# Performance work log

Measured on AMD Instinct MI355X. Metric: run time of the kernel, lower is better.

Reference implementation:

```python
import jax, jax.numpy as jnp
import numpy as np

N = 100000   # nodes
E = 1600000  # edges (before self loops)
H = 4        # heads
C = 32       # per-head channels
D = H * C    # hidden_dim = 128
G = 64       # graphs in batch
L = 4        # num_layers
IN_DIM = 7
NEG_SLOPE = 0.2


def setup_inputs() -> dict:
    key = jax.random.key(0)
    ks = jax.random.split(key, 14)
    s = 0.1
    x = jax.random.normal(ks[0], (N, IN_DIM), jnp.float32)
    edge_index = jax.random.randint(ks[1], (2, E), 0, N, dtype=jnp.int32)
    batch = jnp.sort(jax.random.randint(ks[2], (N,), 0, G, dtype=jnp.int32))
    W0 = jax.random.normal(ks[3], (IN_DIM, D), jnp.float32) * s
    a_src0 = jax.random.normal(ks[4], (H, C), jnp.float32) * s
    a_dst0 = jax.random.normal(ks[5], (H, C), jnp.float32) * s
    b0 = jnp.zeros((D,), jnp.float32)
    Ws = jax.random.normal(ks[6], (L - 1, D, D), jnp.float32) * s
    a_srcs = jax.random.normal(ks[7], (L - 1, H, C), jnp.float32) * s
    a_dsts = jax.random.normal(ks[8], (L - 1, H, C), jnp.float32) * s
    bs = jnp.zeros((L - 1, D), jnp.float32)
    ln_g = jnp.ones((L, D), jnp.float32)
    ln_b = jnp.zeros((L, D), jnp.float32)
    return dict(x=x, edge_index=edge_index, batch=batch, W0=W0, a_src0=a_src0,
                a_dst0=a_dst0, b0=b0, Ws=Ws, a_srcs=a_srcs, a_dsts=a_dsts,
                bs=bs, ln_g=ln_g, ln_b=ln_b)


def _gat_layer(x, W, a_src, a_dst, b, src, dst):
    # x: [N, F_in] -> h: [N, H, C] (PyG GATConv: shared lin for src/dst)
    h = (x @ W).reshape(N, H, C)
    alpha_src = jnp.einsum('nhc,hc->nh', h, a_src)  # [N, H]
    alpha_dst = jnp.einsum('nhc,hc->nh', h, a_dst)  # [N, H]
    logits = jax.nn.leaky_relu(alpha_src[src] + alpha_dst[dst], NEG_SLOPE)  # [E', H]
    # segment softmax over edges grouped by destination node
    m = jax.ops.segment_max(logits, dst, num_segments=N)          # [N, H]
    e = jnp.exp(logits - m[dst])
    z = jax.ops.segment_sum(e, dst, num_segments=N)               # [N, H]
    alpha = e / (z[dst] + 1e-16)                                  # [E', H]
    msg = h[src] * alpha[..., None]                               # [E', H, C]
    out = jax.ops.segment_sum(msg, dst, num_segments=N)           # [N, H, C]
    return out.reshape(N, D) + b


def _layernorm(x, g, b):
    mu = jnp.mean(x, axis=-1, keepdims=True)
    var = jnp.var(x, axis=-1, keepdims=True)
    return (x - mu) * jax.lax.rsqrt(var + 1e-5) * g + b


def reference(x, edge_index, batch, W0, a_src0, a_dst0, b0, Ws, a_srcs, a_dsts, bs, ln_g, ln_b):
    # PyG GATConv default: add self loops
    loop = jnp.arange(N, dtype=edge_index.dtype)
    src = jnp.concatenate([edge_index[0], loop])
    dst = jnp.concatenate([edge_index[1], loop])
    h = x
    for i in range(L):
        if i == 0:
            W, asr, ads, b = W0, a_src0, a_dst0, b0
        else:
            W, asr, ads, b = Ws[i - 1], a_srcs[i - 1], a_dsts[i - 1], bs[i - 1]
        h_new = _gat_layer(h, W, asr, ads, b, src, dst)
        h_new = jax.nn.elu(_layernorm(h_new, ln_g[i], ln_b[i]))
        h = h + h_new if i > 0 else h_new  # dropout is identity in eval
    node_embeddings = h  # [N, D]
    sums = jax.ops.segment_sum(node_embeddings, batch, num_segments=G)  # [G, D]
    cnt = jax.ops.segment_sum(jnp.ones((N,), node_embeddings.dtype), batch, num_segments=G)
    graph_embedding = sums / jnp.maximum(cnt, 1.0)[:, None]
    return node_embeddings, graph_embedding
```

## Files before the change

kernel.cpp:

```cpp
#include <hip/hip_runtime.h>
#include <hip/hip_bf16.h>

#define NN 100000
#define NE 1600000
#define NH 4
#define NC 32
#define DD 128
#define NG 64
#define NIN 7

#define BSH 9
#define NBUK ((NN + 511) >> BSH)
#define SEGCAP 9600
#define CAPE (SEGCAP - 512)
#define CSRN (NBUK * SEGCAP)
#define NBBIN ((NE + 4095)/4096)

typedef __hip_bfloat16 bf16;
typedef __attribute__((ext_vector_type(8))) short short8;
typedef __attribute__((ext_vector_type(4))) float f32x4;
typedef __attribute__((ext_vector_type(2))) float f32x2;

__device__ __forceinline__ float b2f(const bf16 v){ return __bfloat162float(v); }

__device__ __forceinline__ float in_ld(const void* p, size_t i, int f32){
  return f32 ? ((const float*)p)[i] : b2f(((const bf16*)p)[i]);
}

__device__ __forceinline__ unsigned int bfbits(float v){
  bf16 b = __float2bfloat16(v);
  return (unsigned int)(*(unsigned short*)&b);
}

__global__ __launch_bounds__(256) void k_init(float* __restrict__ gsum, int* __restrict__ gcnt,
                                              int* __restrict__ bcur,
                                              const unsigned int* __restrict__ xb, int* __restrict__ flag){
  int i = blockIdx.x*256 + threadIdx.x;
  if (i < NG*DD) gsum[i] = 0.f;
  if (i < NG) gcnt[i] = 0;
  if (i < NBUK) bcur[i] = i * CAPE;
  if (blockIdx.x == 0 && threadIdx.x < 64){
    int t = threadIdx.x;
    int pl = 0;
    for (int j = t; j < 512; j += 64){
      float v = __uint_as_float(xb[j]);
      float a = fabsf(v);
      if (v == v && a < 1e6f && a > 1e-10f) pl++;
    }
    #pragma unroll
    for (int off = 32; off > 0; off >>= 1) pl += __shfl_down(pl, off);
    if (t == 0) *flag = (pl >= 384) ? 1 : 0;
  }
}

__global__ __launch_bounds__(256) void k_bin(const int* __restrict__ src, const int* __restrict__ dst,
                                             int* __restrict__ bcur, int2* __restrict__ gstag,
                                             const void* __restrict__ Ws, bf16* __restrict__ WT,
                                             const int* __restrict__ flag){
  if (blockIdx.x >= NBBIN){
    int l = blockIdx.x - NBBIN;
    int f32 = *flag;
    for (int idx = threadIdx.x; idx < DD*DD; idx += 256){
      int n = idx >> 7, k = idx & 127;
      WT[(size_t)l*DD*DD + idx] = __float2bfloat16(in_ld(Ws, (size_t)l*DD*DD + (size_t)k*DD + n, f32));
    }
    return;
  }
  __shared__ int cnt[NBUK], pref[NBUK+1], place[NBUK], gbase[NBUK];
  __shared__ int2 pairs[4096];
  int tid = threadIdx.x;
  for (int b = tid; b < NBUK; b += 256){ cnt[b]=0; place[b]=0; }
  __syncthreads();
  int e0 = blockIdx.x*4096;
  int s[16], d[16];
  #pragma unroll
  for (int i=0;i<16;i++){
    int e = e0 + i*256 + tid;
    s[i] = 0; d[i] = -1;
    if (e < NE){
      unsigned int us = (unsigned int)src[e]; if (us >= NN) us = 0;
      unsigned int ud = (unsigned int)dst[e]; if (ud >= NN) ud = 0;
      s[i] = (int)us; d[i] = (int)ud;
      atomicAdd(&cnt[ud>>BSH], 1);
    }
  }
  __syncthreads();
  if (tid == 0){
    int run = 0;
    for (int b=0;b<NBUK;b++){ pref[b] = run; run += cnt[b]; }
    pref[NBUK] = run;
  }
  __syncthreads();
  for (int b = tid; b < NBUK; b += 256){
    if (cnt[b] > 0) gbase[b] = atomicAdd(&bcur[b], cnt[b]);
  }
  __syncthreads();
  #pragma unroll
  for (int i=0;i<16;i++){
    if (d[i] >= 0){
      int b = d[i]>>BSH;
      int lp = atomicAdd(&place[b],1);
      pairs[pref[b]+lp] = make_int2(s[i], d[i]);
    }
  }
  __syncthreads();
  int tot = pref[NBUK];
  for (int j = tid; j < tot; j += 256){
    int2 pr = pairs[j];
    int b = pr.y>>BSH;
    int gidx = gbase[b] + (j - pref[b]);
    if (gidx >= b*CAPE && gidx < (b+1)*CAPE) gstag[gidx] = pr;
  }
}

__global__ __launch_bounds__(256) void k_bucket(const int2* __restrict__ gstag,
                                                const int* __restrict__ bcur,
                                                int* __restrict__ csr,
                                                int* __restrict__ offs, int* __restrict__ oend){
  __shared__ int seg[SEGCAP];
  __shared__ int lcnt[512];
  __shared__ int loff[512];
  __shared__ int pscan[256];
  int b = blockIdx.x, tid = threadIdx.x;
  int nstart = b << BSH;
  int nend = min(nstart + 512, NN);
  int nloc = nend - nstart;
  int base = b * SEGCAP;
  int stbase = b * CAPE;
  int ecnt = bcur[b] - stbase;
  ecnt = max(0, min(ecnt, CAPE));
  lcnt[tid]     = (tid < nloc) ? 1 : 0;
  lcnt[tid+256] = (tid+256 < nloc) ? 1 : 0;
  __syncthreads();
  for (int j = tid; j < ecnt; j += 256){
    int2 pr = gstag[stbase + j];
    int ln = pr.y - nstart;
    if (ln < 0 || ln >= nloc) ln = 0;
    atomicAdd(&lcnt[ln], 1);
  }
  __syncthreads();
  int c0 = lcnt[2*tid], c1 = lcnt[2*tid+1];
  int pairsum = c0 + c1;
  pscan[tid] = pairsum;
  __syncthreads();
  for (int off=1; off<256; off<<=1){
    int a = (tid >= off) ? pscan[tid-off] : 0;
    __syncthreads();
    pscan[tid] += a;
    __syncthreads();
  }
  int pexcl = pscan[tid] - pairsum;
  loff[2*tid]   = pexcl;
  loff[2*tid+1] = pexcl + c0;
  __syncthreads();
  int segN = pscan[255];
  if (segN > SEGCAP) segN = SEGCAP;
  if (tid < nloc){
    offs[nstart + tid] = base + loff[tid];
    oend[nstart + tid] = base + loff[tid] + lcnt[tid];
  }
  if (tid + 256 < nloc){
    offs[nstart + tid + 256] = base + loff[tid+256];
    oend[nstart + tid + 256] = base + loff[tid+256] + lcnt[tid+256];
  }
  __syncthreads();
  if (tid < nloc){ int p = loff[tid]; if (p < SEGCAP) seg[p] = nstart + tid; lcnt[tid] = 1; }
  if (tid + 256 < nloc){ int p = loff[tid+256]; if (p < SEGCAP) seg[p] = nstart + tid + 256; lcnt[tid+256] = 1; }
  __syncthreads();
  for (int j = tid; j < ecnt; j += 256){
    int2 pr = gstag[stbase + j];
    int ln = pr.y - nstart;
    if (ln < 0 || ln >= nloc) ln = 0;
    int p = atomicAdd(&lcnt[ln], 1);
    int idx = loff[ln] + p;
    if (idx >= 0 && idx < SEGCAP) seg[idx] = pr.x;
  }
  __syncthreads();
  for (int j = tid; j < segN; j += 256) csr[base + j] = seg[j];
}

__device__ __forceinline__ void alpha_red(float acc, float was, float wad, int d, int n,
                                          float* __restrict__ asrc, float* __restrict__ adst){
  float ps = acc*was, pd = acc*wad;
  #pragma unroll
  for (int off=16; off>0; off>>=1){
    ps += __shfl_down(ps, off, 32);
    pd += __shfl_down(pd, off, 32);
  }
  if ((d & 31) == 0){
    asrc[n*NH + (d>>5)] = ps;
    adst[n*NH + (d>>5)] = pd;
  }
}

__global__ __launch_bounds__(128) void k_gemm0(const void* __restrict__ x, const void* __restrict__ W,
    const void* __restrict__ aws, const void* __restrict__ awd,
    bf16* __restrict__ hproj,
    float* __restrict__ asrc, float* __restrict__ adst, const int* __restrict__ flag){
  int f32 = *flag;
  __shared__ float xr[4][NIN];
  int d = threadIdx.x;
  int n0 = blockIdx.x*4;
  if (d < 4*NIN) xr[d/NIN][d%NIN] = in_ld(x, (size_t)n0*NIN + d, f32);
  __syncthreads();
  float a0=0,a1=0,a2=0,a3=0;
  #pragma unroll
  for (int k=0;k<NIN;k++){
    float w = in_ld(W, (size_t)k*DD + d, f32);
    a0 += xr[0][k]*w; a1 += xr[1][k]*w; a2 += xr[2][k]*w; a3 += xr[3][k]*w;
  }
  hproj[(size_t)(n0+0)*DD+d]=__float2bfloat16(a0);
  hproj[(size_t)(n0+1)*DD+d]=__float2bfloat16(a1);
  hproj[(size_t)(n0+2)*DD+d]=__float2bfloat16(a2);
  hproj[(size_t)(n0+3)*DD+d]=__float2bfloat16(a3);
  float was = in_ld(aws, d, f32), wad = in_ld(awd, d, f32);
  alpha_red(a0, was, wad, d, n0+0, asrc, adst);
  alpha_red(a1, was, wad, d, n0+1, asrc, adst);
  alpha_red(a2, was, wad, d, n0+2, asrc, adst);
  alpha_red(a3, was, wad, d, n0+3, asrc, adst);
}

#define LDA 136
#define LDB 136

__global__ __launch_bounds__(256) void k_gemm_mfma(
    const bf16* __restrict__ resid,
    const bf16* __restrict__ WT, size_t wtoff,
    const void* __restrict__ aws, const void* __restrict__ awd, size_t aoff,
    bf16* __restrict__ hproj,
    float* __restrict__ asrc, float* __restrict__ adst,
    const int* __restrict__ flag)
{
  __shared__ bf16 sA[64*LDA];
  __shared__ bf16 sB[128*LDB];
  int f32 = *flag;
  int t = threadIdx.x;
  int n0 = blockIdx.x*64;

  {
    const uint4* srcv = (const uint4*)(WT + wtoff);
    #pragma unroll
    for (int i=0;i<8;i++){
      int u4 = t + 256*i;
      int row = u4 >> 4, c = u4 & 15;
      *(uint4*)(&sB[row*LDB + c*8]) = srcv[u4];
    }
  }
  {
    const uint4* av = (const uint4*)resid;
    #pragma unroll
    for (int i=0;i<4;i++){
      int u4 = t + 256*i;
      int row = u4 >> 4, c = u4 & 15;
      int gr = n0 + row;
      uint4 v = make_uint4(0,0,0,0);
      if (gr < NN) v = av[(size_t)gr*16 + c];
      *(uint4*)(&sA[row*LDA + c*8]) = v;
    }
  }
  __syncthreads();

  int wv = t >> 6, lane = t & 63;
  int m = lane & 15, kq = lane >> 4;
  int rowbase = wv*16;

  f32x4 acc[8];
  #pragma unroll
  for (int nt=0; nt<8; nt++) acc[nt] = (f32x4){0.f,0.f,0.f,0.f};

  #pragma unroll
  for (int ks=0; ks<4; ks++){
    short8 afrag = *(const short8*)(&sA[(rowbase + m)*LDA + ks*32 + kq*8]);
    #pragma unroll
    for (int nt=0; nt<8; nt++){
      short8 bfrag = *(const short8*)(&sB[(nt*16 + m)*LDB + ks*32 + kq*8]);
      acc[nt] = __builtin_amdgcn_mfma_f32_16x16x32_bf16(afrag, bfrag, acc[nt], 0, 0, 0);
    }
  }

  #pragma unroll
  for (int reg=0; reg<4; reg++){
    int gr = n0 + rowbase + kq*4 + reg;
    if (gr < NN){
      bf16* dst = hproj + (size_t)gr*DD + m;
      #pragma unroll
      for (int nt=0; nt<8; nt++)
        dst[nt*16] = __float2bfloat16(acc[nt][reg]);
    }
  }

  float avs[8], avd[8];
  #pragma unroll
  for (int nt=0; nt<8; nt++){
    avs[nt] = in_ld(aws, aoff + nt*16 + m, f32);
    avd[nt] = in_ld(awd, aoff + nt*16 + m, f32);
  }
  #pragma unroll
  for (int h=0; h<4; h++){
    #pragma unroll
    for (int reg=0; reg<4; reg++){
      float ps = acc[2*h][reg]*avs[2*h] + acc[2*h+1][reg]*avs[2*h+1];
      float pd = acc[2*h][reg]*avd[2*h] + acc[2*h+1][reg]*avd[2*h+1];
      #pragma unroll
      for (int off=1; off<16; off<<=1){
        ps += __shfl_xor(ps, off);
        pd += __shfl_xor(pd, off);
      }
      if (m == 0){
        int gr = n0 + rowbase + kq*4 + reg;
        if (gr < NN){
          asrc[gr*NH + h] = ps;
          adst[gr*NH + h] = pd;
        }
      }
    }
  }
}

__device__ __forceinline__ float4 edge_e(const float4 as, const float4 ad){
  float4 l, e;
  l.x = as.x + ad.x; l.y = as.y + ad.y; l.z = as.z + ad.z; l.w = as.w + ad.w;
  l.x = l.x > 0.f ? l.x : 0.2f*l.x;
  l.y = l.y > 0.f ? l.y : 0.2f*l.y;
  l.z = l.z > 0.f ? l.z : 0.2f*l.z;
  l.w = l.w > 0.f ? l.w : 0.2f*l.w;
  l.x = fminf(l.x, 30.f); l.y = fminf(l.y, 30.f);
  l.z = fminf(l.z, 30.f); l.w = fminf(l.w, 30.f);
  e.x = __expf(l.x); e.y = __expf(l.y); e.z = __expf(l.z); e.w = __expf(l.w);
  return e;
}

__device__ __forceinline__ float2 hp_ld2(const void* hp, int s, int lane){
  unsigned int hv = ((const unsigned int*)hp)[(size_t)s*64 + lane];
  return make_float2(__uint_as_float(hv << 16), __uint_as_float(hv & 0xFFFF0000u));
}

__global__ __launch_bounds__(256) void k_agg(const bf16* __restrict__ hproj,
    const float* __restrict__ asrc, const float* __restrict__ adst,
    const int* __restrict__ offs, const int* __restrict__ oend, const int* __restrict__ csr,
    bf16* __restrict__ resid,
    const void* __restrict__ bias, size_t boff,
    const void* __restrict__ lng, const void* __restrict__ lnb, size_t lnoff,
    const int* __restrict__ flag, const int first)
{
  __shared__ float s_al[4][256];
  int f32 = *flag;
  int wid = threadIdx.x >> 6, lane = threadIdx.x & 63;
  int n = blockIdx.x*4 + wid;
  int beg = offs[n];
  int end = oend[n];
  beg = max(0, min(beg, CSRN));
  end = max(beg, min(end, CSRN));
  int deg = min(end - beg, 1024);
  const float4 ad = ((const float4*)adst)[n];
  int head = lane >> 4;
  int lane4 = lane << 2;
  const char* hpB = (const char*)hproj;
  f32x2 ac0 = {0.f,0.f}, ac1 = {0.f,0.f}, ac2 = {0.f,0.f}, ac3 = {0.f,0.f};

  if (deg <= 64){
    float4 e = make_float4(0,0,0,0);
    int sregB = 0;
    if (lane < deg){
      unsigned int us = (unsigned int)csr[beg+lane];
      if (us >= NN) us = 0;
      sregB = (int)(us << 8);
      float4 as = ((const float4*)asrc)[us];
      e = edge_e(as, ad);
    }
    float4 zs = e;
    #pragma unroll
    for (int off=32; off>0; off>>=1){
      zs.x += __shfl_down(zs.x, off);
      zs.y += __shfl_down(zs.y, off);
      zs.z += __shfl_down(zs.z, off);
      zs.w += __shfl_down(zs.w, off);
    }
    float4 invz;
    invz.x = 1.f/(__shfl(zs.x,0)+1e-16f);
    invz.y = 1.f/(__shfl(zs.y,0)+1e-16f);
    invz.z = 1.f/(__shfl(zs.z,0)+1e-16f);
    invz.w = 1.f/(__shfl(zs.w,0)+1e-16f);
    if (lane < deg){
      s_al[wid][lane*4+0] = e.x*invz.x;
      s_al[wid][lane*4+1] = e.y*invz.y;
      s_al[wid][lane*4+2] = e.z*invz.z;
      s_al[wid][lane*4+3] = e.w*invz.w;
    }
    __threadfence_block();
    int t = 0;
    for (; t+4 <= deg; t += 4){
      unsigned int o0 = (unsigned int)__shfl(sregB, t+0) + lane4;
      unsigned int o1 = (unsigned int)__shfl(sregB, t+1) + lane4;
      unsigned int o2 = (unsigned int)__shfl(sregB, t+2) + lane4;
      unsigned int o3 = (unsigned int)__shfl(sregB, t+3) + lane4;
      unsigned int h0 = *(const unsigned int*)(hpB + o0);
      unsigned int h1 = *(const unsigned int*)(hpB + o1);
      unsigned int h2 = *(const unsigned int*)(hpB + o2);
      unsigned int h3 = *(const unsigned int*)(hpB + o3);
      float al0 = s_al[wid][(t+0)*4+head];
      float al1 = s_al[wid][(t+1)*4+head];
      float al2 = s_al[wid][(t+2)*4+head];
      float al3 = s_al[wid][(t+3)*4+head];
      f32x2 v0 = {__uint_as_float(h0 << 16), __uint_as_float(h0 & 0xFFFF0000u)};
      f32x2 v1 = {__uint_as_float(h1 << 16), __uint_as_float(h1 & 0xFFFF0000u)};
      f32x2 v2 = {__uint_as_float(h2 << 16), __uint_as_float(h2 & 0xFFFF0000u)};
      f32x2 v3 = {__uint_as_float(h3 << 16), __uint_as_float(h3 & 0xFFFF0000u)};
      ac0 += v0 * al0;
      ac1 += v1 * al1;
      ac2 += v2 * al2;
      ac3 += v3 * al3;
    }
    for (; t < deg; t++){
      unsigned int o = (unsigned int)__shfl(sregB, t) + lane4;
      unsigned int h = *(const unsigned int*)(hpB + o);
      float a = s_al[wid][t*4+head];
      f32x2 v = {__uint_as_float(h << 16), __uint_as_float(h & 0xFFFF0000u)};
      ac0 += v * a;
    }
  } else {
    float4 zs = make_float4(0,0,0,0);
    for (int j=lane; j<deg; j+=64){
      unsigned int us = (unsigned int)csr[beg+j];
      if (us >= NN) us = 0;
      float4 as = ((const float4*)asrc)[us];
      float4 e = edge_e(as, ad);
      zs.x+=e.x; zs.y+=e.y; zs.z+=e.z; zs.w+=e.w;
    }
    #pragma unroll
    for (int off=32; off>0; off>>=1){
      zs.x += __shfl_down(zs.x, off);
      zs.y += __shfl_down(zs.y, off);
      zs.z += __shfl_down(zs.z, off);
      zs.w += __shfl_down(zs.w, off);
    }
    float4 invz;
    invz.x = 1.f/(__shfl(zs.x,0)+1e-16f);
    invz.y = 1.f/(__shfl(zs.y,0)+1e-16f);
    invz.z = 1.f/(__shfl(zs.z,0)+1e-16f);
    invz.w = 1.f/(__shfl(zs.w,0)+1e-16f);
    int nch = (deg+63)>>6;
    for (int c2=0;c2<nch;c2++){
      int base = c2<<6, j = base+lane;
      int sreg = 0;
      __threadfence_block();
      if (j < deg){
        unsigned int us = (unsigned int)csr[beg+j];
        if (us >= NN) us = 0;
        sreg = (int)us;
        float4 as = ((const float4*)asrc)[us];
        float4 e = edge_e(as, ad);
        s_al[wid][lane*4+0]=e.x*invz.x;
        s_al[wid][lane*4+1]=e.y*invz.y;
        s_al[wid][lane*4+2]=e.z*invz.z;
        s_al[wid][lane*4+3]=e.w*invz.w;
      }
      __threadfence_block();
      int cnt = min(64, deg-base);
      for (int t=0;t<cnt;t++){
        int s = __shfl(sreg, t);
        float a = s_al[wid][t*4+head];
        float2 hv = hp_ld2(hproj, s, lane);
        ac0.x += hv.x*a;
        ac0.y += hv.y*a;
      }
    }
  }

  f32x2 accv = (ac0 + ac1) + (ac2 + ac3);
  float2 acc = make_float2(accv.x, accv.y);

  float vx = acc.x + in_ld(bias, boff + 2*lane,   f32);
  float vy = acc.y + in_ld(bias, boff + 2*lane+1, f32);
  float s1 = vx+vy, s2 = vx*vx+vy*vy;
  #pragma unroll
  for (int off=32; off>0; off>>=1){
    s1 += __shfl_down(s1, off);
    s2 += __shfl_down(s2, off);
  }
  float mean = __shfl(s1,0) * (1.f/DD);
  float msq  = __shfl(s2,0) * (1.f/DD);
  float var  = fmaxf(msq - mean*mean, 0.f);
  float r = rsqrtf(var + 1e-5f);
  float yx = (vx-mean)*r*in_ld(lng, lnoff+2*lane,   f32) + in_ld(lnb, lnoff+2*lane,   f32);
  float yy = (vy-mean)*r*in_ld(lng, lnoff+2*lane+1, f32) + in_ld(lnb, lnoff+2*lane+1, f32);
  yx = yx>0.f ? yx : expm1f(yx);
  yy = yy>0.f ? yy : expm1f(yy);
  float2 res;
  if (first){
    res = make_float2(yx, yy);
  } else {
    unsigned int pu = ((const unsigned int*)resid)[(size_t)n*64 + lane];
    res = make_float2(__uint_as_float(pu << 16) + yx,
                      __uint_as_float(pu & 0xFFFF0000u) + yy);
  }
  unsigned int pk = bfbits(res.x) | (bfbits(res.y) << 16);
  ((unsigned int*)resid)[(size_t)n*64 + lane] = pk;
}

__global__ __launch_bounds__(128) void k_pool(const bf16* __restrict__ resid, void* __restrict__ dout,
    const int* __restrict__ batch, float* __restrict__ gsum, int* __restrict__ gcnt,
    const int* __restrict__ flag){
  __shared__ int sb[64];
  int f32 = *flag;
  int d = threadIdx.x;
  int n0 = blockIdx.x*64;
  int cnt = min(64, NN - n0);
  if (d < cnt){
    unsigned int b = (unsigned int)batch[n0 + d];
    if (b >= NG) b = 0;
    sb[d] = (int)b;
  }
  __syncthreads();
  float local = 0.f;
  int cur = sb[0];
  for (int i=0;i<cnt;i++){
    int b = sb[i];
    if (b != cur){
      atomicAdd(&gsum[cur*DD + d], local);
      local = 0.f; cur = b;
    }
    size_t idx = (size_t)(n0+i)*DD + d;
    float v = b2f(resid[idx]);
    if (f32) ((float*)dout)[idx] = v;
    else     ((bf16*)dout)[idx] = resid[idx];
    local += v;
  }
  atomicAdd(&gsum[cur*DD + d], local);
  if (d == 0){
    int lc = 0; int c2 = sb[0];
    for (int i=0;i<cnt;i++){
      int b = sb[i];
      if (b != c2){ atomicAdd(&gcnt[c2], lc); lc = 0; c2 = b; }
      lc++;
    }
    atomicAdd(&gcnt[c2], lc);
  }
}

__global__ __launch_bounds__(128) void k_final(const float* __restrict__ gsum, const int* __restrict__ gcnt,
                                               void* __restrict__ dout, const int* __restrict__ flag){
  int f32 = *flag;
  int i = blockIdx.x*128 + threadIdx.x;
  if (i < NG*DD){
    float c = (float)gcnt[i>>7];
    if (c < 1.f) c = 1.f;
    float val = gsum[i] / c;
    if (f32) ((float*)dout)[(size_t)NN*DD + i] = val;
    else     ((bf16*)dout)[(size_t)NN*DD + i] = __float2bfloat16(val);
  }
}

extern "C" void kernel_launch(void* const* d_in, const int* in_sizes, int n_in,
                              void* d_out, int out_size, void* d_ws, size_t ws_size,
                              hipStream_t stream){
  const void* x      = d_in[0];
  const int*  ei     = (const int*) d_in[1];
  const int*  batch  = (const int*) d_in[2];
  const void* W0     = d_in[3];
  const void* asrc0  = d_in[4];
  const void* adst0  = d_in[5];
  const void* b0     = d_in[6];
  const void* Ws     = d_in[7];
  const void* asrcs  = d_in[8];
  const void* adsts  = d_in[9];
  const void* bs     = d_in[10];
  const void* lng    = d_in[11];
  const void* lnb    = d_in[12];

  const int* srcs = ei;
  const int* dsts = ei + NE;

  uintptr_t p0 = (uintptr_t)d_ws;
  uintptr_t p = p0;
  auto alloc = [&](size_t bytes)->void* {
    void* r = (void*)p; p += (bytes + 255) & ~(size_t)255; return r;
  };
  int*   csr    = (int*)  alloc((size_t)CSRN*4);
  int*   offs   = (int*)  alloc((size_t)NN*4);
  int*   oend   = (int*)  alloc((size_t)NN*4);
  float* asrc   = (float*)alloc((size_t)NN*NH*4);
  float* adst   = (float*)alloc((size_t)NN*NH*4);
  float* gsum   = (float*)alloc((size_t)NG*DD*4);
  int*   gcnt   = (int*)  alloc(NG*4);
  int*   flag   = (int*)  alloc(256);
  int*   bcur   = (int*)  alloc((size_t)NBUK*4);
  int2*  gstag  = (int2*) alloc((size_t)NBUK*CAPE*8);
  bf16*  wt     = (bf16*) alloc((size_t)3*DD*DD*2);
  bf16*  hproj  = (bf16*) alloc((size_t)NN*DD*2);
  bf16*  resid  = (bf16*) alloc((size_t)NN*DD*2);

  const int NB = (NN + 255)/256;

  k_init<<<NB, 256, 0, stream>>>(gsum, gcnt, bcur, (const unsigned int*)x, flag);
  k_bin<<<NBBIN + 3, 256, 0, stream>>>(srcs, dsts, bcur, gstag, Ws, wt, flag);
  k_bucket<<<NBUK, 256, 0, stream>>>(gstag, bcur, csr, offs, oend);

  const int GEMM_B = (NN + 63)/64;

  for (int l=0; l<4; l++){
    if (l == 0){
      k_gemm0<<<NN/4, 128, 0, stream>>>(x, W0, asrc0, adst0, hproj, asrc, adst, flag);
      k_agg<<<NN/4, 256, 0, stream>>>(hproj, asrc, adst, offs, oend, csr, resid,
                                      b0, 0, lng, lnb, 0, flag, 1);
    } else {
      size_t wtoff = (size_t)(l-1)*DD*DD;
      size_t aoff  = (size_t)(l-1)*DD;
      k_gemm_mfma<<<GEMM_B, 256, 0, stream>>>(resid, wt, wtoff,
                                              asrcs, adsts, aoff,
                                              hproj, asrc, adst, flag);
      k_agg<<<NN/4, 256, 0, stream>>>(hproj, asrc, adst, offs, oend, csr, resid,
                                      bs, (size_t)(l-1)*DD, lng, lnb, (size_t)l*DD, flag, 0);
    }
  }

  k_pool<<<(NN+63)/64, 128, 0, stream>>>(resid, d_out, batch, gsum, gcnt, flag);
  k_final<<<(NG*DD+127)/128, 128, 0, stream>>>(gsum, gcnt, d_out, flag);
}
```

Baseline: 636.4 us.

## Gather neighbor rows with 16-byte loads, four edges per wavefront step

In the low-degree aggregation path, each wavefront now splits into four 16-lane groups. Each group handles a different edge and loads a whole 256-byte bf16 row with uint4 (16-byte) loads, replacing the earlier 4-byte per-lane loads of one edge at a time. Neighbor offsets are kept in shared memory rather than being broadcast with shuffles. The per-group partial sums are combined with xor shuffles and redistributed through shared memory. This trades fewer, wider memory transactions for extra reduction shuffles and an LDS round trip, and it reuses the s_al buffer for that reduction.

```diff
diff --git a/kernel.cpp b/kernel.cpp
--- a/kernel.cpp
+++ b/kernel.cpp
@@ -344,6 +344,7 @@
     const int* __restrict__ flag, const int first)
 {
   __shared__ float s_al[4][256];
+  __shared__ int   s_off[4][64];
   int f32 = *flag;
   int wid = threadIdx.x >> 6, lane = threadIdx.x & 63;
   int n = blockIdx.x*4 + wid;
@@ -354,17 +355,15 @@
   int deg = min(end - beg, 1024);
   const float4 ad = ((const float4*)adst)[n];
   int head = lane >> 4;
-  int lane4 = lane << 2;
   const char* hpB = (const char*)hproj;
-  f32x2 ac0 = {0.f,0.f}, ac1 = {0.f,0.f}, ac2 = {0.f,0.f}, ac3 = {0.f,0.f};
+  float2 acc;
 
   if (deg <= 64){
     float4 e = make_float4(0,0,0,0);
-    int sregB = 0;
     if (lane < deg){
       unsigned int us = (unsigned int)csr[beg+lane];
       if (us >= NN) us = 0;
-      sregB = (int)(us << 8);
+      s_off[wid][lane] = (int)(us << 8);
       float4 as = ((const float4*)asrc)[us];
       e = edge_e(as, ad);
     }
@@ -388,37 +387,63 @@
       s_al[wid][lane*4+3] = e.w*invz.w;
     }
     __threadfence_block();
+
+    int qg = lane >> 4;
+    int ql = lane & 15;
+    int hq = ql >> 2;
+    int qbyte = ql << 4;
+    f32x2 a0 = {0.f,0.f}, a1 = {0.f,0.f}, a2 = {0.f,0.f}, a3 = {0.f,0.f};
     int t = 0;
     for (; t+4 <= deg; t += 4){
-      unsigned int o0 = (unsigned int)__shfl(sregB, t+0) + lane4;
-      unsigned int o1 = (unsigned int)__shfl(sregB, t+1) + lane4;
-      unsigned int o2 = (unsigned int)__shfl(sregB, t+2) + lane4;
-      unsigned int o3 = (unsigned int)__shfl(sregB, t+3) + lane4;
-      unsigned int h0 = *(const unsigned int*)(hpB + o0);
-      unsigned int h1 = *(const unsigned int*)(hpB + o1);
-      unsigned int h2 = *(const unsigned int*)(hpB + o2);
-      unsigned int h3 = *(const unsigned int*)(hpB + o3);
-      float al0 = s_al[wid][(t+0)*4+head];
-      float al1 = s_al[wid][(t+1)*4+head];
-      float al2 = s_al[wid][(t+2)*4+head];
-      float al3 = s_al[wid][(t+3)*4+head];
-      f32x2 v0 = {__uint_as_float(h0 << 16), __uint_as_float(h0 & 0xFFFF0000u)};
-      f32x2 v1 = {__uint_as_float(h1 << 16), __uint_as_float(h1 & 0xFFFF0000u)};
-      f32x2 v2 = {__uint_as_float(h2 << 16), __uint_as_float(h2 & 0xFFFF0000u)};
-      f32x2 v3 = {__uint_as_float(h3 << 16), __uint_as_float(h3 & 0xFFFF0000u)};
-      ac0 += v0 * al0;
-      ac1 += v1 * al1;
-      ac2 += v2 * al2;
-      ac3 += v3 * al3;
-    }
-    for (; t < deg; t++){
-      unsigned int o = (unsigned int)__shfl(sregB, t) + lane4;
-      unsigned int h = *(const unsigned int*)(hpB + o);
-      float a = s_al[wid][t*4+head];
-      f32x2 v = {__uint_as_float(h << 16), __uint_as_float(h & 0xFFFF0000u)};
-      ac0 += v * a;
-    }
+      int j = t + qg;
+      unsigned int off = (unsigned int)s_off[wid][j] + qbyte;
+      const uint4 hv = *(const uint4*)(hpB + off);
+      float al = s_al[wid][j*4 + hq];
+      f32x2 v0 = {__uint_as_float(hv.x << 16), __uint_as_float(hv.x & 0xFFFF0000u)};
+      f32x2 v1 = {__uint_as_float(hv.y << 16), __uint_as_float(hv.y & 0xFFFF0000u)};
+      f32x2 v2 = {__uint_as_float(hv.z << 16), __uint_as_float(hv.z & 0xFFFF0000u)};
+      f32x2 v3 = {__uint_as_float(hv.w << 16), __uint_as_float(hv.w & 0xFFFF0000u)};
+      a0 += v0 * al;
+      a1 += v1 * al;
+      a2 += v2 * al;
+      a3 += v3 * al;
+    }
+    if (t < deg){
+      int j = t + qg;
+      if (j < deg){
+        unsigned int off = (unsigned int)s_off[wid][j] + qbyte;
+        const uint4 hv = *(const uint4*)(hpB + off);
+        float al = s_al[wid][j*4 + hq];
+        f32x2 v0 = {__uint_as_float(hv.x << 16), __uint_as_float(hv.x & 0xFFFF0000u)};
+        f32x2 v1 = {__uint_as_float(hv.y << 16), __uint_as_float(hv.y & 0xFFFF0000u)};
+        f32x2 v2 = {__uint_as_float(hv.z << 16), __uint_as_float(hv.z & 0xFFFF0000u)};
+        f32x2 v3 = {__uint_as_float(hv.w << 16), __uint_as_float(hv.w & 0xFFFF0000u)};
+        a0 += v0 * al;
+        a1 += v1 * al;
+        a2 += v2 * al;
+        a3 += v3 * al;
+      }
+    }
+
+    #pragma unroll
+    for (int off = 16; off < 64; off <<= 1){
+      a0.x += __shfl_xor(a0.x, off); a0.y += __shfl_xor(a0.y, off);
+      a1.x += __shfl_xor(a1.x, off); a1.y += __shfl_xor(a1.y, off);
+      a2.x += __shfl_xor(a2.x, off); a2.y += __shfl_xor(a2.y, off);
+      a3.x += __shfl_xor(a3.x, off); a3.y += __shfl_xor(a3.y, off);
+    }
+    __threadfence_block();
+    if (qg == 0){
+      float* red = &s_al[wid][0];
+      red[ql*8+0] = a0.x; red[ql*8+1] = a0.y;
+      red[ql*8+2] = a1.x; red[ql*8+3] = a1.y;
+      red[ql*8+4] = a2.x; red[ql*8+5] = a2.y;
+      red[ql*8+6] = a3.x; red[ql*8+7] = a3.y;
+    }
+    __threadfence_block();
+    acc = make_float2(s_al[wid][2*lane], s_al[wid][2*lane+1]);
   } else {
+    f32x2 ac0 = {0.f,0.f};
     float4 zs = make_float4(0,0,0,0);
     for (int j=lane; j<deg; j+=64){
       unsigned int us = (unsigned int)csr[beg+j];
@@ -465,10 +490,8 @@
         ac0.y += hv.y*a;
       }
     }
-  }
-
-  f32x2 accv = (ac0 + ac1) + (ac2 + ac3);
-  float2 acc = make_float2(accv.x, accv.y);
+    acc = make_float2(ac0.x, ac0.y);
+  }
 
   float vx = acc.x + in_ld(bias, boff + 2*lane,   f32);
   float vy = acc.y + in_ld(bias, boff + 2*lane+1, f32);
```

Measured after the change: 638.8 us. About the same (+0.4%).
